# Kernel optimization log

Measured on AMD Instinct MI355X. Metric: run time of the kernel, lower is better.

## Reference

```python
import jax, jax.numpy as jnp
import numpy as np

NUM_HEADS = 12


def setup_inputs() -> dict:
    key = jax.random.key(0)
    ks = jax.random.split(key, 6)
    C = 768
    hd = C // NUM_HEADS  # 64
    H = W = 32
    x = jax.random.normal(ks[0], (4, H, W, C), dtype=jnp.float32)
    # Linear weights stored as (in, out) so y = x @ W (+ b)
    Wqkv = jax.random.normal(ks[1], (C, 3 * C), dtype=jnp.float32) * 0.02
    Wproj = jax.random.normal(ks[2], (C, C), dtype=jnp.float32) * 0.02
    bproj = jax.random.normal(ks[3], (C,), dtype=jnp.float32) * 0.02
    rel_pos_h = jax.random.normal(ks[4], (2 * H - 1, hd), dtype=jnp.float32) * 0.02
    rel_pos_w = jax.random.normal(ks[5], (2 * W - 1, hd), dtype=jnp.float32) * 0.02
    return {"x": x, "Wqkv": Wqkv, "Wproj": Wproj, "bproj": bproj,
            "rel_pos_h": rel_pos_h, "rel_pos_w": rel_pos_w}


def _get_rel_pos(size: int, rel_pos: jnp.ndarray) -> jnp.ndarray:
    # q_size == k_size == size; table already has 2*size-1 entries -> no interpolation
    coords = jnp.arange(size)[:, None] - jnp.arange(size)[None, :] + (size - 1)
    return rel_pos[coords]  # (size, size, head_dim)


def reference(x, Wqkv, Wproj, bproj, rel_pos_h, rel_pos_w):
    B, H, W, C = x.shape
    hn = NUM_HEADS
    hd = C // hn
    scale = hd ** (-0.5)
    S = H * W

    qkv = x @ Wqkv                                   # (B,H,W,3C)
    qkv = qkv.reshape(B, S, 3, hn, hd)
    qkv = jnp.transpose(qkv, (2, 0, 3, 1, 4)).reshape(3, B * hn, S, hd)
    q, k, v = qkv[0], qkv[1], qkv[2]                 # each (B*hn, S, hd)

    # decomposed relative position bias
    Rh = _get_rel_pos(H, rel_pos_h)                  # (H,H,hd)
    Rw = _get_rel_pos(W, rel_pos_w)                  # (W,W,hd)
    r_q = q.reshape(B * hn, H, W, hd)
    rel_h = jnp.einsum('bhwc,hkc->bhwk', r_q, Rh)    # (B*hn,H,W,H)
    rel_w = jnp.einsum('bhwc,wkc->bhwk', r_q, Rw)    # (B*hn,H,W,W)
    bias = rel_h[..., :, None] + rel_w[..., None, :] # (B*hn,H,W,H,W)
    bias = bias.reshape(B * hn, S, S)

    scores = scale * jnp.einsum('bqc,bkc->bqk', q, k) + bias
    attn = jax.nn.softmax(scores, axis=-1)
    out = jnp.einsum('bqk,bkc->bqc', attn, v)        # (B*hn,S,hd)

    out = out.reshape(B, hn, H, W, hd)
    out = jnp.transpose(out, (0, 2, 3, 1, 4)).reshape(B, H, W, C)
    return out @ Wproj + bproj
```

## Files before the change

### kernel.cpp

```cpp
#include <hip/hip_runtime.h>
#include <stddef.h>

typedef __bf16 bf16x8 __attribute__((ext_vector_type(8)));
typedef __bf16 bf16x4 __attribute__((ext_vector_type(4)));
typedef _Float16 f16x4 __attribute__((ext_vector_type(4)));
typedef float  f32x4  __attribute__((ext_vector_type(4)));

#define MFMA16(a, b, c) __builtin_amdgcn_mfma_f32_16x16x32_bf16((a), (b), (c), 0, 0, 0)
#define MFMA16H(a, b, c) __builtin_amdgcn_mfma_f32_16x16x16f16((a), (b), (c), 0, 0, 0)

__device__ __forceinline__ void gload_lds16(const void* gsrc, void* ldst) {
    __builtin_amdgcn_global_load_lds(
        (__attribute__((address_space(1))) void*)gsrc,
        (__attribute__((address_space(3))) void*)ldst,
        16, 0, 0);
}

__global__ void prep_kernel(const float* __restrict__ x, __bf16* __restrict__ xbf,
                            const float* __restrict__ Wqkv, __bf16* __restrict__ WqkvT,
                            const float* __restrict__ Wproj, __bf16* __restrict__ WprojT) {
    __shared__ float tile[32][33];
    const int bx = blockIdx.x, tid = threadIdx.x;
    if (bx < 3072) {
        int i = bx * 256 + tid;
        float4 v = ((const float4*)x)[i];
        bf16x4 o = {(__bf16)v.x, (__bf16)v.y, (__bf16)v.z, (__bf16)v.w};
        ((bf16x4*)xbf)[i] = o;
        return;
    }
    const float* in; __bf16* out; int R, C, c0, r0;
    if (bx < 4800) { int bb = bx - 3072; in = Wqkv;  out = WqkvT;  R = 768; C = 2304;
                     c0 = (bb % 72) * 32; r0 = (bb / 72) * 32; }
    else           { int bb = bx - 4800; in = Wproj; out = WprojT; R = 768; C = 768;
                     c0 = (bb % 24) * 32; r0 = (bb / 24) * 32; }
    const int tx = tid & 31, ty = tid >> 5;
#pragma unroll
    for (int i = 0; i < 32; i += 8)
        tile[ty + i][tx] = in[(size_t)(r0 + ty + i) * C + c0 + tx];
    __syncthreads();
#pragma unroll
    for (int i = 0; i < 32; i += 8)
        out[(size_t)(c0 + ty + i) * R + r0 + tx] = (__bf16)tile[tx][ty + i];
}

template<int BM, int BN>
__device__ __forceinline__ void gemm_core_bk64(
    const __bf16* __restrict__ A, const __bf16* __restrict__ Bt, int K,
    int m0, int n0, __bf16* aT, __bf16* bT, f32x4 (&acc)[BM/32][BN/32]) {
    const int tid  = threadIdx.x;
    const int wid  = tid >> 6, lane = tid & 63;
    const int quad = lane >> 4, l16 = lane & 15;
    const int wm = (wid >> 1) * (BM / 2), wn = (wid & 1) * (BN / 2);
    const int r_in = lane >> 3;
    const int cswz = ((lane & 7) ^ r_in) * 8;
    const __bf16* gA = A  + (size_t)(m0 + wid * 8 + r_in) * K + cswz;
    const __bf16* gB = Bt + (size_t)(n0 + wid * 8 + r_in) * K + cswz;
    const int sA = (l16 & 7);
    for (int k0 = 0; k0 < K; k0 += 64) {
        __syncthreads();
#pragma unroll
        for (int j = 0; j < BM / 32; j++)
            gload_lds16(gA + (size_t)(j * 32) * K + k0, aT + (j * 32 + wid * 8) * 64);
#pragma unroll
        for (int j = 0; j < BN / 32; j++)
            gload_lds16(gB + (size_t)(j * 32) * K + k0, bT + (j * 32 + wid * 8) * 64);
        __syncthreads();
#pragma unroll
        for (int kh = 0; kh < 2; kh++) {
            bf16x8 af[BM / 32], bfr[BN / 32];
            const int slot = ((kh * 4 + quad) ^ sA) << 3;
#pragma unroll
            for (int t = 0; t < BM / 32; t++)
                af[t]  = *(const bf16x8*)(aT + (wm + t * 16 + l16) * 64 + slot);
#pragma unroll
            for (int t = 0; t < BN / 32; t++)
                bfr[t] = *(const bf16x8*)(bT + (wn + t * 16 + l16) * 64 + slot);
#pragma unroll
            for (int rt = 0; rt < BM / 32; rt++)
#pragma unroll
                for (int ct = 0; ct < BN / 32; ct++)
                    acc[rt][ct] = MFMA16(af[rt], bfr[ct], acc[rt][ct]);
        }
    }
}

__global__ __launch_bounds__(256, 3)
void gemm_qkv_kernel(const __bf16* __restrict__ A, const __bf16* __restrict__ Bt,
                     __bf16* __restrict__ qb, __bf16* __restrict__ kb,
                     _Float16* __restrict__ vtb) {
    __shared__ __bf16 aT[8192], bT[6144];
    f32x4 acc[4][3];
#pragma unroll
    for (int i = 0; i < 4; i++)
#pragma unroll
        for (int j = 0; j < 3; j++) { f32x4 z = {0.f, 0.f, 0.f, 0.f}; acc[i][j] = z; }
    const int m0 = blockIdx.x * 128, n0 = blockIdx.y * 96;
    gemm_core_bk64<128, 96>(A, Bt, 768, m0, n0, aT, bT, acc);
    const int tid = threadIdx.x, wid = tid >> 6, lane = tid & 63;
    const int quad = lane >> 4, l16 = lane & 15;
    const int wm = (wid >> 1) * 64, wn = (wid & 1) * 48;
#pragma unroll
    for (int rt = 0; rt < 4; rt++)
#pragma unroll
        for (int ct = 0; ct < 3; ct++) {
            const int ng = n0 + wn + ct * 16 + l16;
            const int which = ng / 768;
            const int rem = ng - which * 768;
            const int hh = rem >> 6, d = rem & 63;
#pragma unroll
            for (int r = 0; r < 4; r++) {
                const int mg = m0 + wm + rt * 16 + quad * 4 + r;
                const int b = mg >> 10, s = mg & 1023;
                const int bh = b * 12 + hh;
                if (which == 0)      qb[((size_t)bh * 1024 + s) * 64 + d] = (__bf16)acc[rt][ct][r];
                else if (which == 1) kb[((size_t)bh * 1024 + s) * 64 + d] = (__bf16)acc[rt][ct][r];
                else                 vtb[((size_t)bh * 64 + d) * 1024 + s] = (_Float16)acc[rt][ct][r];
            }
        }
}

__global__ __launch_bounds__(256, 3)
void gemm_proj_kernel(const __bf16* __restrict__ A, const __bf16* __restrict__ Bt,
                      const float* __restrict__ bias, float* __restrict__ out) {
    __shared__ __bf16 aT[4096], bT[6144];
    f32x4 acc[2][3];
#pragma unroll
    for (int i = 0; i < 2; i++)
#pragma unroll
        for (int j = 0; j < 3; j++) { f32x4 z = {0.f, 0.f, 0.f, 0.f}; acc[i][j] = z; }
    const int m0 = blockIdx.x * 64, n0 = blockIdx.y * 96;
    gemm_core_bk64<64, 96>(A, Bt, 768, m0, n0, aT, bT, acc);
    const int tid = threadIdx.x, wid = tid >> 6, lane = tid & 63;
    const int quad = lane >> 4, l16 = lane & 15;
    const int wm = (wid >> 1) * 32, wn = (wid & 1) * 48;
#pragma unroll
    for (int rt = 0; rt < 2; rt++)
#pragma unroll
        for (int ct = 0; ct < 3; ct++) {
            const int ng = n0 + wn + ct * 16 + l16;
            const float bb = bias[ng];
#pragma unroll
            for (int r = 0; r < 4; r++) {
                const int mg = m0 + wm + rt * 16 + quad * 4 + r;
                out[(size_t)mg * 768 + ng] = acc[rt][ct][r] + bb;
            }
        }
}

__global__ __launch_bounds__(256, 3)
void attn_kernel(const __bf16* __restrict__ q, const __bf16* __restrict__ kk,
                 const _Float16* __restrict__ vt, const float* __restrict__ rph,
                 const float* __restrict__ rpw, __bf16* __restrict__ aout) {
    __shared__ __bf16   kbuf2[2][4096];
    __shared__ _Float16 vbuf2[2][4096];
    __shared__ float    relh[64][33];
    const int tid = threadIdx.x, wid = tid >> 6, lane = tid & 63;
    const int quad = lane >> 4, l16 = lane & 15;
    const int bh = blockIdx.x, qt = blockIdx.y;
    const int b = bh / 12, hh = bh - b * 12;
    const int q0 = qt * 64;
    const int w0 = wid * 16;
    const int h = qt * 2 + (wid >> 1);

    const __bf16* qp = q + ((size_t)bh * 1024 + q0 + w0 + l16) * 64;
    bf16x8 aq0 = *(const bf16x8*)(qp + quad * 8);
    bf16x8 aq1 = *(const bf16x8*)(qp + 32 + quad * 8);

    float* Dw = ((float*)kbuf2) + wid * 1024;
#pragma unroll
    for (int ct = 0; ct < 4; ct++) {
        int j = ct * 16 + l16; if (j > 62) j = 62;
        const float* tb = rpw + (size_t)j * 64;
        float4 t0 = *(const float4*)(tb + quad * 8);
        float4 t1 = *(const float4*)(tb + quad * 8 + 4);
        float4 t2 = *(const float4*)(tb + 32 + quad * 8);
        float4 t3 = *(const float4*)(tb + 32 + quad * 8 + 4);
        bf16x8 b0 = {(__bf16)t0.x, (__bf16)t0.y, (__bf16)t0.z, (__bf16)t0.w,
                     (__bf16)t1.x, (__bf16)t1.y, (__bf16)t1.z, (__bf16)t1.w};
        bf16x8 b1 = {(__bf16)t2.x, (__bf16)t2.y, (__bf16)t2.z, (__bf16)t2.w,
                     (__bf16)t3.x, (__bf16)t3.y, (__bf16)t3.z, (__bf16)t3.w};
        f32x4 z = {0.f, 0.f, 0.f, 0.f};
        z = MFMA16(aq0, b0, z);
        z = MFMA16(aq1, b1, z);
#pragma unroll
        for (int i = 0; i < 4; i++)
            Dw[(quad * 4 + i) * 64 + ct * 16 + l16] = z[i];
    }
#pragma unroll
    for (int ct = 0; ct < 2; ct++) {
        const int tr = h - (ct * 16 + l16) + 31;
        const float* tb = rph + (size_t)tr * 64;
        float4 t0 = *(const float4*)(tb + quad * 8);
        float4 t1 = *(const float4*)(tb + quad * 8 + 4);
        float4 t2 = *(const float4*)(tb + 32 + quad * 8);
        float4 t3 = *(const float4*)(tb + 32 + quad * 8 + 4);
        bf16x8 b0 = {(__bf16)t0.x, (__bf16)t0.y, (__bf16)t0.z, (__bf16)t0.w,
                     (__bf16)t1.x, (__bf16)t1.y, (__bf16)t1.z, (__bf16)t1.w};
        bf16x8 b1 = {(__bf16)t2.x, (__bf16)t2.y, (__bf16)t2.z, (__bf16)t2.w,
                     (__bf16)t3.x, (__bf16)t3.y, (__bf16)t3.z, (__bf16)t3.w};
        f32x4 z = {0.f, 0.f, 0.f, 0.f};
        z = MFMA16(aq0, b0, z);
        z = MFMA16(aq1, b1, z);
#pragma unroll
        for (int i = 0; i < 4; i++)
            relh[w0 + quad * 4 + i][ct * 16 + l16] = z[i];
    }
    const int wq = (wid & 1) * 16 + l16;
    float bw[2][4];
#pragma unroll
    for (int hf = 0; hf < 2; hf++)
#pragma unroll
        for (int r = 0; r < 4; r++)
            bw[hf][r] = Dw[l16 * 64 + wq + 31 - hf * 16 - quad * 4 - r];
    __syncthreads();

    float l_run = 0.f;
    f32x4 o_acc[4];
#pragma unroll
    for (int t = 0; t < 4; t++) { f32x4 z = {0.f, 0.f, 0.f, 0.f}; o_acc[t] = z; }

    const __bf16*   kg0 = kk + (size_t)bh * 65536;
    const _Float16* vg0 = vt + (size_t)bh * 65536;
    const int cbase = wid * 2;
    const int srow = lane >> 3;
    const int scol = ((lane & 7) ^ srow) * 8;
    const int swz0 = ((quad ^ (l16 & 7)) << 3);
    const int swz1 = (((quad | 4) ^ (l16 & 7)) << 3);
    const int l7 = l16 & 7, qhi = quad >> 1, qlo = (quad & 1) * 4;

    auto stage = [&](int buf, int kt) {
        const __bf16*   kg = kg0 + kt * 4096;
        const _Float16* vg = vg0 + kt * 64;
        __bf16*   kb_ = &kbuf2[buf][0];
        _Float16* vb_ = &vbuf2[buf][0];
#pragma unroll
        for (int j = 0; j < 2; j++) {
            const int c = cbase + j;
            gload_lds16(kg + (c * 8 + srow) * 64 + scol, kb_ + c * 512);
            gload_lds16(vg + (size_t)(c * 8 + srow) * 1024 + scol, vb_ + c * 512);
        }
    };

    stage(0, 0);
    for (int kt = 0; kt < 16; kt++) {
        const int cur = kt & 1;
        __syncthreads();
        if (kt < 15) stage(1 - cur, kt + 1);
        const __bf16*   kbuf = &kbuf2[cur][0];
        const _Float16* vbuf = &vbuf2[cur][0];

        f32x4 sacc[4];
#pragma unroll
        for (int ct = 0; ct < 4; ct++) {
            const int key = ct * 16 + l16;
            bf16x8 bk0 = *(const bf16x8*)(kbuf + key * 64 + swz0);
            bf16x8 bk1 = *(const bf16x8*)(kbuf + key * 64 + swz1);
            f32x4 z = {0.f, 0.f, 0.f, 0.f};
            z = MFMA16(bk0, aq0, z);
            z = MFMA16(bk1, aq1, z);
            sacc[ct] = z;
        }

        const float bh0 = relh[w0 + l16][kt * 2];
        const float bh1 = relh[w0 + l16][kt * 2 + 1];
        f16x4 pf[4];
#pragma unroll
        for (int ct = 0; ct < 4; ct++) {
            const float bhc = (ct < 2) ? bh0 : bh1;
#pragma unroll
            for (int r = 0; r < 4; r++) {
                float sv = fmaf(sacc[ct][r], 0.125f, bhc + bw[ct & 1][r]);
                float p = __expf(sv);
                l_run += p;
                pf[ct][r] = (_Float16)p;
            }
        }

#pragma unroll
        for (int dt = 0; dt < 4; dt++) {
            const int vrow = (dt * 16 + l16) * 64;
#pragma unroll
            for (int ct = 0; ct < 4; ct++) {
                const int slot = (ct * 2 + qhi) ^ l7;
                f16x4 vf = *(const f16x4*)(vbuf + vrow + slot * 8 + qlo);
                o_acc[dt] = MFMA16H(vf, pf[ct], o_acc[dt]);
            }
        }
    }

    l_run += __shfl_xor(l_run, 16);
    l_run += __shfl_xor(l_run, 32);
    const float inv = 1.f / l_run;
    const int srow_o = q0 + w0 + l16;
#pragma unroll
    for (int dt = 0; dt < 4; dt++) {
        bf16x4 ov = {(__bf16)(o_acc[dt][0] * inv), (__bf16)(o_acc[dt][1] * inv),
                     (__bf16)(o_acc[dt][2] * inv), (__bf16)(o_acc[dt][3] * inv)};
        *(bf16x4*)&aout[((size_t)b * 1024 + srow_o) * 768 + hh * 64 + dt * 16 + quad * 4] = ov;
    }
}

extern "C" void kernel_launch(void* const* d_in, const int* in_sizes, int n_in,
                              void* d_out, int out_size, void* d_ws, size_t ws_size,
                              hipStream_t stream) {
    const float* x     = (const float*)d_in[0];
    const float* Wqkv  = (const float*)d_in[1];
    const float* Wproj = (const float*)d_in[2];
    const float* bproj = (const float*)d_in[3];
    const float* rph   = (const float*)d_in[4];
    const float* rpw   = (const float*)d_in[5];
    float* out = (float*)d_out;
    char* ws = (char*)d_ws;

    __bf16*   xbf    = (__bf16*)(ws);
    __bf16*   WqkvT  = (__bf16*)(ws + 6291456);
    __bf16*   WprojT = (__bf16*)(ws + 9830400);
    __bf16*   qb     = (__bf16*)(ws + 11010048);
    __bf16*   kb     = (__bf16*)(ws + 17301504);
    _Float16* vtb    = (_Float16*)(ws + 23592960);
    __bf16*   aob    = (__bf16*)(ws + 29884416);

    prep_kernel<<<dim3(5376), dim3(256), 0, stream>>>(x, xbf, Wqkv, WqkvT, Wproj, WprojT);
    gemm_qkv_kernel<<<dim3(32, 24), dim3(256), 0, stream>>>(xbf, WqkvT, qb, kb, vtb);
    attn_kernel<<<dim3(48, 16), dim3(256), 0, stream>>>(qb, kb, vtb, rph, rpw, aob);
    gemm_proj_kernel<<<dim3(64, 8), dim3(256), 0, stream>>>(aob, WprojT, bproj, out);
}
```

Before: 141.8 us.

## Split attention key tiles across wave pairs with 2x2 query-key register blocking

After: 143.9 us. About the same (+1.5%).

```diff
diff --git a/kernel.cpp b/kernel.cpp
--- a/kernel.cpp
+++ b/kernel.cpp
@@ -156,17 +156,28 @@
     __shared__ float    relh[64][33];
     const int tid = threadIdx.x, wid = tid >> 6, lane = tid & 63;
     const int quad = lane >> 4, l16 = lane & 15;
+    const int qh = wid & 1, kp = wid >> 1;
     const int bh = blockIdx.x, qt = blockIdx.y;
     const int b = bh / 12, hh = bh - b * 12;
     const int q0 = qt * 64;
     const int w0 = wid * 16;
     const int h = qt * 2 + (wid >> 1);
-
-    const __bf16* qp = q + ((size_t)bh * 1024 + q0 + w0 + l16) * 64;
-    bf16x8 aq0 = *(const bf16x8*)(qp + quad * 8);
-    bf16x8 aq1 = *(const bf16x8*)(qp + 32 + quad * 8);
-
-    float* Dw = ((float*)kbuf2) + wid * 1024;
+    const float LOG2E = 1.44269504f;
+
+    const __bf16* qpa = q + ((size_t)bh * 1024 + q0 + w0 + l16) * 64;
+    bf16x8 aqA0 = *(const bf16x8*)(qpa + quad * 8);
+    bf16x8 aqA1 = *(const bf16x8*)(qpa + 32 + quad * 8);
+
+    bf16x8 aq[2][2];
+#pragma unroll
+    for (int gi = 0; gi < 2; gi++) {
+        const __bf16* qpg = q + ((size_t)bh * 1024 + q0 + qh * 32 + gi * 16 + l16) * 64;
+        aq[gi][0] = *(const bf16x8*)(qpg + quad * 8);
+        aq[gi][1] = *(const bf16x8*)(qpg + 32 + quad * 8);
+    }
+
+    float* DwAll = (float*)kbuf2;
+    float* Dw = DwAll + wid * 1024;
 #pragma unroll
     for (int ct = 0; ct < 4; ct++) {
         int j = ct * 16 + l16; if (j > 62) j = 62;
@@ -175,13 +186,13 @@
         float4 t1 = *(const float4*)(tb + quad * 8 + 4);
         float4 t2 = *(const float4*)(tb + 32 + quad * 8);
         float4 t3 = *(const float4*)(tb + 32 + quad * 8 + 4);
-        bf16x8 b0 = {(__bf16)t0.x, (__bf16)t0.y, (__bf16)t0.z, (__bf16)t0.w,
-                     (__bf16)t1.x, (__bf16)t1.y, (__bf16)t1.z, (__bf16)t1.w};
-        bf16x8 b1 = {(__bf16)t2.x, (__bf16)t2.y, (__bf16)t2.z, (__bf16)t2.w,
-                     (__bf16)t3.x, (__bf16)t3.y, (__bf16)t3.z, (__bf16)t3.w};
+        bf16x8 b0 = {(__bf16)(t0.x*LOG2E), (__bf16)(t0.y*LOG2E), (__bf16)(t0.z*LOG2E), (__bf16)(t0.w*LOG2E),
+                     (__bf16)(t1.x*LOG2E), (__bf16)(t1.y*LOG2E), (__bf16)(t1.z*LOG2E), (__bf16)(t1.w*LOG2E)};
+        bf16x8 b1 = {(__bf16)(t2.x*LOG2E), (__bf16)(t2.y*LOG2E), (__bf16)(t2.z*LOG2E), (__bf16)(t2.w*LOG2E),
+                     (__bf16)(t3.x*LOG2E), (__bf16)(t3.y*LOG2E), (__bf16)(t3.z*LOG2E), (__bf16)(t3.w*LOG2E)};
         f32x4 z = {0.f, 0.f, 0.f, 0.f};
-        z = MFMA16(aq0, b0, z);
-        z = MFMA16(aq1, b1, z);
+        z = MFMA16(aqA0, b0, z);
+        z = MFMA16(aqA1, b1, z);
 #pragma unroll
         for (int i = 0; i < 4; i++)
             Dw[(quad * 4 + i) * 64 + ct * 16 + l16] = z[i];
@@ -194,30 +205,36 @@
         float4 t1 = *(const float4*)(tb + quad * 8 + 4);
         float4 t2 = *(const float4*)(tb + 32 + quad * 8);
         float4 t3 = *(const float4*)(tb + 32 + quad * 8 + 4);
-        bf16x8 b0 = {(__bf16)t0.x, (__bf16)t0.y, (__bf16)t0.z, (__bf16)t0.w,
-                     (__bf16)t1.x, (__bf16)t1.y, (__bf16)t1.z, (__bf16)t1.w};
-        bf16x8 b1 = {(__bf16)t2.x, (__bf16)t2.y, (__bf16)t2.z, (__bf16)t2.w,
-                     (__bf16)t3.x, (__bf16)t3.y, (__bf16)t3.z, (__bf16)t3.w};
+        bf16x8 b0 = {(__bf16)(t0.x*LOG2E), (__bf16)(t0.y*LOG2E), (__bf16)(t0.z*LOG2E), (__bf16)(t0.w*LOG2E),
+                     (__bf16)(t1.x*LOG2E), (__bf16)(t1.y*LOG2E), (__bf16)(t1.z*LOG2E), (__bf16)(t1.w*LOG2E)};
+        bf16x8 b1 = {(__bf16)(t2.x*LOG2E), (__bf16)(t2.y*LOG2E), (__bf16)(t2.z*LOG2E), (__bf16)(t2.w*LOG2E),
+                     (__bf16)(t3.x*LOG2E), (__bf16)(t3.y*LOG2E), (__bf16)(t3.z*LOG2E), (__bf16)(t3.w*LOG2E)};
         f32x4 z = {0.f, 0.f, 0.f, 0.f};
-        z = MFMA16(aq0, b0, z);
-        z = MFMA16(aq1, b1, z);
+        z = MFMA16(aqA0, b0, z);
+        z = MFMA16(aqA1, b1, z);
 #pragma unroll
         for (int i = 0; i < 4; i++)
             relh[w0 + quad * 4 + i][ct * 16 + l16] = z[i];
     }
-    const int wq = (wid & 1) * 16 + l16;
-    float bw[2][4];
-#pragma unroll
-    for (int hf = 0; hf < 2; hf++)
-#pragma unroll
-        for (int r = 0; r < 4; r++)
-            bw[hf][r] = Dw[l16 * 64 + wq + 31 - hf * 16 - quad * 4 - r];
-    __syncthreads();
-
-    float l_run = 0.f;
-    f32x4 o_acc[4];
-#pragma unroll
-    for (int t = 0; t < 4; t++) { f32x4 z = {0.f, 0.f, 0.f, 0.f}; o_acc[t] = z; }
+    __syncthreads();
+
+    float bw[2][2][4];
+#pragma unroll
+    for (int gi = 0; gi < 2; gi++)
+#pragma unroll
+        for (int ctl = 0; ctl < 2; ctl++)
+#pragma unroll
+            for (int r = 0; r < 4; r++)
+                bw[gi][ctl][r] = DwAll[(qh * 2 + gi) * 1024 + l16 * 64 +
+                                       gi * 16 + l16 + 31 - ctl * 16 - quad * 4 - r];
+    __syncthreads();
+
+    float l_part[2] = {0.f, 0.f};
+    f32x4 o_acc[4][2];
+#pragma unroll
+    for (int t = 0; t < 4; t++)
+#pragma unroll
+        for (int gi = 0; gi < 2; gi++) { f32x4 z = {0.f, 0.f, 0.f, 0.f}; o_acc[t][gi] = z; }
 
     const __bf16*   kg0 = kk + (size_t)bh * 65536;
     const _Float16* vg0 = vt + (size_t)bh * 65536;
@@ -249,54 +266,90 @@
         const __bf16*   kbuf = &kbuf2[cur][0];
         const _Float16* vbuf = &vbuf2[cur][0];
 
-        f32x4 sacc[4];
-#pragma unroll
-        for (int ct = 0; ct < 4; ct++) {
-            const int key = ct * 16 + l16;
+        f32x4 sacc[2][2];
+#pragma unroll
+        for (int ctl = 0; ctl < 2; ctl++) {
+            const int key = kp * 32 + ctl * 16 + l16;
             bf16x8 bk0 = *(const bf16x8*)(kbuf + key * 64 + swz0);
             bf16x8 bk1 = *(const bf16x8*)(kbuf + key * 64 + swz1);
-            f32x4 z = {0.f, 0.f, 0.f, 0.f};
-            z = MFMA16(bk0, aq0, z);
-            z = MFMA16(bk1, aq1, z);
-            sacc[ct] = z;
-        }
-
-        const float bh0 = relh[w0 + l16][kt * 2];
-        const float bh1 = relh[w0 + l16][kt * 2 + 1];
-        f16x4 pf[4];
-#pragma unroll
-        for (int ct = 0; ct < 4; ct++) {
-            const float bhc = (ct < 2) ? bh0 : bh1;
-#pragma unroll
-            for (int r = 0; r < 4; r++) {
-                float sv = fmaf(sacc[ct][r], 0.125f, bhc + bw[ct & 1][r]);
-                float p = __expf(sv);
-                l_run += p;
-                pf[ct][r] = (_Float16)p;
-            }
+#pragma unroll
+            for (int gi = 0; gi < 2; gi++) {
+                f32x4 z = {0.f, 0.f, 0.f, 0.f};
+                z = MFMA16(bk0, aq[gi][0], z);
+                z = MFMA16(bk1, aq[gi][1], z);
+                sacc[ctl][gi] = z;
+            }
+        }
+
+        f16x4 pf[2][2];
+#pragma unroll
+        for (int gi = 0; gi < 2; gi++) {
+            const float bhc = relh[(qh * 2 + gi) * 16 + l16][kt * 2 + kp];
+#pragma unroll
+            for (int ctl = 0; ctl < 2; ctl++)
+#pragma unroll
+                for (int r = 0; r < 4; r++) {
+                    float sv = fmaf(sacc[ctl][gi][r], 0.18033688f, bhc + bw[gi][ctl][r]);
+                    float p = __builtin_amdgcn_exp2f(sv);
+                    l_part[gi] += p;
+                    pf[ctl][gi][r] = (_Float16)p;
+                }
         }
 
 #pragma unroll
         for (int dt = 0; dt < 4; dt++) {
             const int vrow = (dt * 16 + l16) * 64;
 #pragma unroll
-            for (int ct = 0; ct < 4; ct++) {
-                const int slot = (ct * 2 + qhi) ^ l7;
+            for (int ctl = 0; ctl < 2; ctl++) {
+                const int c = kp * 4 + ctl * 2 + qhi;
+                const int slot = c ^ l7;
                 f16x4 vf = *(const f16x4*)(vbuf + vrow + slot * 8 + qlo);
-                o_acc[dt] = MFMA16H(vf, pf[ct], o_acc[dt]);
-            }
-        }
-    }
-
-    l_run += __shfl_xor(l_run, 16);
-    l_run += __shfl_xor(l_run, 32);
-    const float inv = 1.f / l_run;
-    const int srow_o = q0 + w0 + l16;
-#pragma unroll
-    for (int dt = 0; dt < 4; dt++) {
-        bf16x4 ov = {(__bf16)(o_acc[dt][0] * inv), (__bf16)(o_acc[dt][1] * inv),
-                     (__bf16)(o_acc[dt][2] * inv), (__bf16)(o_acc[dt][3] * inv)};
-        *(bf16x4*)&aout[((size_t)b * 1024 + srow_o) * 768 + hh * 64 + dt * 16 + quad * 4] = ov;
+#pragma unroll
+                for (int gi = 0; gi < 2; gi++)
+                    o_acc[dt][gi] = MFMA16H(vf, pf[ctl][gi], o_acc[dt][gi]);
+            }
+        }
+    }
+
+    __syncthreads();
+
+    float* lred = &relh[0][0];
+#pragma unroll
+    for (int gi = 0; gi < 2; gi++) {
+        float s = l_part[gi];
+        s += __shfl_xor(s, 16);
+        s += __shfl_xor(s, 32);
+        if (quad == 0) lred[(wid * 2 + gi) * 16 + l16] = s;
+    }
+    float* ored = (float*)kbuf2;
+    if (kp == 1) {
+#pragma unroll
+        for (int dt = 0; dt < 4; dt++)
+#pragma unroll
+            for (int gi = 0; gi < 2; gi++)
+                *(f32x4*)(ored + qh * 2048 + (dt * 2 + gi) * 256 + quad * 64 + l16 * 4)
+                    = o_acc[dt][gi];
+    }
+    __syncthreads();
+    if (kp == 0) {
+        float linv[2];
+#pragma unroll
+        for (int gi = 0; gi < 2; gi++)
+            linv[gi] = 1.f / (lred[(qh * 2 + gi) * 16 + l16] +
+                              lred[(4 + qh * 2 + gi) * 16 + l16]);
+#pragma unroll
+        for (int dt = 0; dt < 4; dt++)
+#pragma unroll
+            for (int gi = 0; gi < 2; gi++) {
+                f32x4 p = *(const f32x4*)(ored + qh * 2048 + (dt * 2 + gi) * 256 +
+                                          quad * 64 + l16 * 4);
+                f32x4 o = o_acc[dt][gi] + p;
+                bf16x4 ov = {(__bf16)(o[0] * linv[gi]), (__bf16)(o[1] * linv[gi]),
+                             (__bf16)(o[2] * linv[gi]), (__bf16)(o[3] * linv[gi])};
+                const int srow_o = q0 + (qh * 2 + gi) * 16 + l16;
+                *(bf16x4*)&aout[((size_t)b * 1024 + srow_o) * 768 + hh * 64 +
+                                dt * 16 + quad * 4] = ov;
+            }
     }
 }
 
```
